# Performance work log

Hardware: AMD Instinct MI355X
Metric: run time of the kernel (lower is better)

The kernel has to match this reference:

```python
import jax, jax.numpy as jnp
import numpy as np

VOC, EMB, HID = 32000, 1024, 1024
B, S = 32, 128


def setup_inputs() -> dict:
    key = jax.random.key(0)
    ks = jax.random.split(key, 12)
    s_e = 1.0 / np.sqrt(EMB)
    s_h = 1.0 / np.sqrt(HID)
    return {
        "inputs": jax.random.randint(ks[0], (B, S), 0, VOC, dtype=jnp.int64),
        "emb": jax.random.normal(ks[1], (VOC, EMB), jnp.float32),
        "W_ih1": jax.random.uniform(ks[2], (4 * HID, EMB), jnp.float32, -s_h, s_h),
        "W_hh1": jax.random.uniform(ks[3], (4 * HID, HID), jnp.float32, -s_h, s_h),
        "b_ih1": jax.random.uniform(ks[4], (4 * HID,), jnp.float32, -s_h, s_h),
        "b_hh1": jax.random.uniform(ks[5], (4 * HID,), jnp.float32, -s_h, s_h),
        "W_ih2": jax.random.uniform(ks[6], (4 * HID, HID), jnp.float32, -s_h, s_h),
        "W_hh2": jax.random.uniform(ks[7], (4 * HID, HID), jnp.float32, -s_h, s_h),
        "b_ih2": jax.random.uniform(ks[8], (4 * HID,), jnp.float32, -s_h, s_h),
        "b_hh2": jax.random.uniform(ks[9], (4 * HID,), jnp.float32, -s_h, s_h),
        "W_out": jax.random.uniform(ks[10], (VOC, HID), jnp.float32, -s_h, s_h),
        "b_out": jnp.zeros((VOC,), jnp.float32),  # init_weights zeroes logits bias
    }


def _lstm_cell(x, h, c, W_ih, W_hh, b_ih, b_hh):
    # torch LSTMCell gate order: i, f, g, o
    gates = x @ W_ih.T + b_ih + h @ W_hh.T + b_hh  # [B, 4H]
    i, f, g, o = jnp.split(gates, 4, axis=-1)
    c_new = jax.nn.sigmoid(f) * c + jax.nn.sigmoid(i) * jnp.tanh(g)
    h_new = jax.nn.sigmoid(o) * jnp.tanh(c_new)
    return h_new, c_new


def reference(inputs, emb, W_ih1, W_hh1, b_ih1, b_hh1, W_ih2, W_hh2, b_ih2, b_hh2, W_out, b_out):
    embed = emb[inputs]  # [B, S, E]
    bsz = embed.shape[0]
    hid = W_hh1.shape[1]
    init = (jnp.zeros((bsz, hid), embed.dtype), jnp.zeros((bsz, hid), embed.dtype),
            jnp.zeros((bsz, hid), embed.dtype), jnp.zeros((bsz, hid), embed.dtype))

    def step(carry, x_t):
        h1, c1, h2, c2 = carry
        h1, c1 = _lstm_cell(x_t, h1, c1, W_ih1, W_hh1, b_ih1, b_hh1)
        h2, c2 = _lstm_cell(h1, h2, c2, W_ih2, W_hh2, b_ih2, b_hh2)  # dropout = identity (eval)
        return (h1, c1, h2, c2), h2

    _, hid_seq = jax.lax.scan(step, init, jnp.swapaxes(embed, 0, 1))  # [S, B, H]
    hid_seq = jnp.swapaxes(hid_seq, 0, 1)  # [B, S, H]
    logits = hid_seq @ W_out.T + b_out  # [B, S, V]
    return jax.nn.log_softmax(logits, axis=-1)
```

## Files before the change

### kernel.cpp

```cpp
#include <hip/hip_runtime.h>


#define SEQ   128
#define NBAT  32
#define HID   1024
#define VOC   32000

typedef __attribute__((ext_vector_type(4))) float        f32x4;
typedef __attribute__((ext_vector_type(4))) unsigned int u32x4;
typedef __attribute__((ext_vector_type(2))) unsigned int u32x2;

__device__ __forceinline__ unsigned short f2bf(float f) {
    unsigned u = __builtin_bit_cast(unsigned, f);
    u += 0x7fffu + ((u >> 16) & 1u);
    return (unsigned short)(u >> 16);
}
__device__ __forceinline__ unsigned pk2(float a, float b) {
    return (unsigned)f2bf(a) | ((unsigned)f2bf(b) << 16);
}
__device__ __forceinline__ void mfma16(f32x4& d, u32x4 a, u32x4 b) {
    asm("v_mfma_f32_16x16x32_bf16 %0, %1, %2, %0" : "+v"(d) : "v"(a), "v"(b));
}
__device__ __forceinline__ void mfma_fence() {
    __builtin_amdgcn_sched_barrier(0);
    asm volatile("s_nop 7\ns_nop 7\ns_nop 7");
    __builtin_amdgcn_sched_barrier(0);
}

__global__ void cast_bf16_k(const float* __restrict__ in,
                            unsigned short* __restrict__ out, int n4) {
    int i = blockIdx.x * blockDim.x + threadIdx.x;
    int stride = gridDim.x * blockDim.x;
    for (; i < n4; i += stride) {
        f32x4 v = ((const f32x4*)in)[i];
        u32x2 p = { pk2(v.x, v.y), pk2(v.z, v.w) };
        ((u32x2*)out)[i] = p;
    }
}

__global__ void gather_k(const int* __restrict__ tok, const float* __restrict__ emb,
                         unsigned short* __restrict__ xe) {
    int row = blockIdx.x;
    int t   = tok[row];
    const f32x4* src = (const f32x4*)(emb + (size_t)t * HID);
    u32x2*       dst = (u32x2*)(xe + (size_t)row * HID);
    int i = threadIdx.x;
    f32x4 v = src[i];
    u32x2 p = { pk2(v.x, v.y), pk2(v.z, v.w) };
    dst[i] = p;
}

template<bool BF32>
__global__ __launch_bounds__(256, 2) void gemm_k(
    const unsigned short* __restrict__ A, const void* __restrict__ Bsrc,
    const float* __restrict__ bias1, const float* __restrict__ bias2,
    float* __restrict__ C, int N)
{
    __shared__ u32x4 As[128][8];
    __shared__ u32x4 Bs[128][8];
    const int tid  = threadIdx.x;
    const int lane = tid & 63, wid = tid >> 6;
    const int wm = (wid >> 1) * 64, wn = (wid & 1) * 64;
    const int m0 = blockIdx.x * 128, n0 = blockIdx.y * 128;
    const int r = tid >> 1, half = tid & 1;
    f32x4 acc[4][4] = {};

    const unsigned short* Ar = A + (size_t)(m0 + r) * HID + half * 32;
    for (int kt = 0; kt < HID / 64; ++kt) {
        const int k0 = kt * 64;
        {
            const u32x4* s = (const u32x4*)(Ar + k0);
            #pragma unroll
            for (int c = 0; c < 4; ++c)
                As[r][(half * 4 + c) ^ (r & 7)] = s[c];
        }
        if constexpr (!BF32) {
            const u32x4* s = (const u32x4*)((const unsigned short*)Bsrc +
                              (size_t)(n0 + r) * HID + half * 32 + k0);
            #pragma unroll
            for (int c = 0; c < 4; ++c)
                Bs[r][(half * 4 + c) ^ (r & 7)] = s[c];
        } else {
            const f32x4* s = (const f32x4*)((const float*)Bsrc +
                              (size_t)(n0 + r) * HID + half * 32 + k0);
            #pragma unroll
            for (int c = 0; c < 4; ++c) {
                f32x4 v0 = s[2 * c], v1 = s[2 * c + 1];
                u32x4 p = { pk2(v0.x, v0.y), pk2(v0.z, v0.w),
                            pk2(v1.x, v1.y), pk2(v1.z, v1.w) };
                Bs[r][(half * 4 + c) ^ (r & 7)] = p;
            }
        }
        __syncthreads();
        #pragma unroll
        for (int h = 0; h < 2; ++h) {
            u32x4 af[4], bfr[4];
            #pragma unroll
            for (int i = 0; i < 4; ++i) {
                int ra = wm + i * 16 + (lane & 15);
                af[i]  = As[ra][(h * 4 + (lane >> 4)) ^ (ra & 7)];
                int rb = wn + i * 16 + (lane & 15);
                bfr[i] = Bs[rb][(h * 4 + (lane >> 4)) ^ (rb & 7)];
            }
            #pragma unroll
            for (int i = 0; i < 4; ++i)
                #pragma unroll
                for (int j = 0; j < 4; ++j)
                    mfma16(acc[i][j], af[i], bfr[j]);
        }
        __syncthreads();
    }
    mfma_fence();
    #pragma unroll
    for (int j = 0; j < 4; ++j) {
        int col = n0 + wn + j * 16 + (lane & 15);
        float bv = 0.f;
        if (bias1) bv += bias1[col];
        if (bias2) bv += bias2[col];
        #pragma unroll
        for (int i = 0; i < 4; ++i) {
            int mrow = m0 + wm + i * 16 + (lane >> 4) * 4;
            #pragma unroll
            for (int q = 0; q < 4; ++q)
                C[(size_t)(mrow + q) * N + col] = acc[i][j][q] + bv;
        }
    }
}

__global__ __launch_bounds__(256, 2) void lstm_k(
    const float* __restrict__ X, const unsigned short* __restrict__ Whh,
    unsigned short* __restrict__ hseq, float* __restrict__ cst, int t)
{
    __shared__ u32x4 hl[32][128];
    __shared__ float gl[4][32][16];
    const int tid  = threadIdx.x;
    const int lane = tid & 63, wid = tid >> 6;
    const int u0 = blockIdx.x * 16;
    f32x4 acc0 = {}, acc1 = {};

    if (t > 0) {
        const int b = tid >> 3;
        const u32x4* src = (const u32x4*)(hseq + (size_t)(b * SEQ + t - 1) * HID);
        #pragma unroll
        for (int q = 0; q < 16; ++q) {
            int c = (tid & 7) + q * 8;
            hl[b][c ^ (b & 7)] = src[c];
        }
        __syncthreads();
        const unsigned short* Wr = Whh + (size_t)(wid * HID + u0 + (lane & 15)) * HID
                                       + (lane >> 4) * 8;
        #pragma unroll 8
        for (int ks = 0; ks < 32; ++ks) {
            u32x4 bf = *(const u32x4*)(Wr + ks * 32);
            u32x4 a0 = hl[lane & 15][(ks * 4 + (lane >> 4)) ^ (lane & 7)];
            u32x4 a1 = hl[16 + (lane & 15)][(ks * 4 + (lane >> 4)) ^ (lane & 7)];
            mfma16(acc0, a0, bf);
            mfma16(acc1, a1, bf);
        }
    }
    mfma_fence();
    #pragma unroll
    for (int q = 0; q < 4; ++q) {
        gl[wid][(lane >> 4) * 4 + q][lane & 15]      = acc0[q];
        gl[wid][16 + (lane >> 4) * 4 + q][lane & 15] = acc1[q];
    }
    __syncthreads();
    #pragma unroll
    for (int p = tid; p < 512; p += 256) {
        const int b = p >> 4, u = p & 15;
        const float* Xr = X + (size_t)(b * SEQ + t) * (4 * HID) + u0 + u;
        float ig = gl[0][b][u] + Xr[0];
        float fg = gl[1][b][u] + Xr[HID];
        float gg = gl[2][b][u] + Xr[2 * HID];
        float og = gl[3][b][u] + Xr[3 * HID];
        float cp = (t == 0) ? 0.f : cst[b * HID + u0 + u];
        float si = 1.f / (1.f + __expf(-ig));
        float sf = 1.f / (1.f + __expf(-fg));
        float so = 1.f / (1.f + __expf(-og));
        float tg = tanhf(gg);
        float cn = sf * cp + si * tg;
        float hn = so * tanhf(cn);
        cst[b * HID + u0 + u] = cn;
        hseq[(size_t)(b * SEQ + t) * HID + u0 + u] = f2bf(hn);
    }
}

__global__ __launch_bounds__(256) void lsm_k(float* __restrict__ out) {
    const int tid = threadIdx.x;
    float* p = out + (size_t)blockIdx.x * VOC;
    float m = -1e30f, s = 0.f;
    for (int i = tid; i < VOC / 4; i += 256) {
        f32x4 v = ((const f32x4*)p)[i];
        float vm = fmaxf(fmaxf(v.x, v.y), fmaxf(v.z, v.w));
        if (vm > m) { s *= __expf(m - vm); m = vm; }
        s += __expf(v.x - m) + __expf(v.y - m) + __expf(v.z - m) + __expf(v.w - m);
    }
    #pragma unroll
    for (int o = 32; o; o >>= 1) {
        float om = __shfl_xor(m, o), os = __shfl_xor(s, o);
        float M = fmaxf(m, om);
        s = s * __expf(m - M) + os * __expf(om - M);
        m = M;
    }
    __shared__ float rm[4], rs[4];
    if ((tid & 63) == 0) { rm[tid >> 6] = m; rs[tid >> 6] = s; }
    __syncthreads();
    float M = fmaxf(fmaxf(rm[0], rm[1]), fmaxf(rm[2], rm[3]));
    float S = rs[0] * __expf(rm[0] - M) + rs[1] * __expf(rm[1] - M)
            + rs[2] * __expf(rm[2] - M) + rs[3] * __expf(rm[3] - M);
    float lse = M + logf(S);
    for (int i = tid; i < VOC / 4; i += 256) {
        f32x4 v = ((const f32x4*)p)[i];
        v.x -= lse; v.y -= lse; v.z -= lse; v.w -= lse;
        ((f32x4*)p)[i] = v;
    }
}

extern "C" void kernel_launch(void* const* d_in, const int* in_sizes, int n_in,
                              void* d_out, int out_size, void* d_ws, size_t ws_size,
                              hipStream_t stream)
{
    (void)in_sizes; (void)n_in; (void)out_size; (void)ws_size;
    const int*   tok  = (const int*)d_in[0];
    const float* emb  = (const float*)d_in[1];
    const float* Wih1 = (const float*)d_in[2];
    const float* Whh1 = (const float*)d_in[3];
    const float* bih1 = (const float*)d_in[4];
    const float* bhh1 = (const float*)d_in[5];
    const float* Wih2 = (const float*)d_in[6];
    const float* Whh2 = (const float*)d_in[7];
    const float* bih2 = (const float*)d_in[8];
    const float* bhh2 = (const float*)d_in[9];
    const float* Wout = (const float*)d_in[10];
    const float* bout = (const float*)d_in[11];
    float* out = (float*)d_out;
    char*  ws  = (char*)d_ws;

    unsigned short* Wih1b = (unsigned short*)(ws + (0ull  << 20));
    unsigned short* Whh1b = (unsigned short*)(ws + (8ull  << 20));
    unsigned short* Wih2b = (unsigned short*)(ws + (16ull << 20));
    unsigned short* Whh2b = (unsigned short*)(ws + (24ull << 20));
    unsigned short* Xemb  = (unsigned short*)(ws + (32ull << 20));
    unsigned short* h1s   = (unsigned short*)(ws + (40ull << 20));
    unsigned short* h2s   = (unsigned short*)(ws + (48ull << 20));
    float* c1 = (float*)(ws + (56ull << 20));
    float* c2 = (float*)(ws + (56ull << 20) + (1ull << 19));
    float* X1 = out;
    float* X2 = out + (16ull << 20);

    const int n4w = (4 * HID * HID) / 4;
    cast_bf16_k<<<1024, 256, 0, stream>>>(Wih1, Wih1b, n4w);
    cast_bf16_k<<<1024, 256, 0, stream>>>(Whh1, Whh1b, n4w);
    cast_bf16_k<<<1024, 256, 0, stream>>>(Wih2, Wih2b, n4w);
    cast_bf16_k<<<1024, 256, 0, stream>>>(Whh2, Whh2b, n4w);
    gather_k<<<NBAT * SEQ, 256, 0, stream>>>(tok, emb, Xemb);

    gemm_k<false><<<dim3(32, 32), 256, 0, stream>>>(Xemb, Wih1b, bih1, bhh1, X1, 4 * HID);
    for (int t = 0; t < SEQ; ++t)
        lstm_k<<<64, 256, 0, stream>>>(X1, Whh1b, h1s, c1, t);

    gemm_k<false><<<dim3(32, 32), 256, 0, stream>>>(h1s, Wih2b, bih2, bhh2, X2, 4 * HID);
    for (int t = 0; t < SEQ; ++t)
        lstm_k<<<64, 256, 0, stream>>>(X2, Whh2b, h2s, c2, t);

    gemm_k<true><<<dim3(32, VOC / 128), 256, 0, stream>>>(h2s, Wout, bout, nullptr, out, VOC);
    lsm_k<<<NBAT * SEQ, 256, 0, stream>>>(out);
}
```

Measured before the change: 3.677 ms.

## Replace per-timestep LSTM launches with persistent kernel and grid barrier

Each LSTM layer's 128 per-timestep launches are replaced by one persistent kernel of 128 blocks that loops over time, synchronised by an atomic counter grid barrier. Each block keeps its W_hh slice in registers as bf16, casting from fp32 at kernel start, so the separate W_hh cast kernels go away. The cell state stays in a register and h is read straight from global memory instead of being staged through LDS. This targets launch overhead and repeated weight reloads. In exchange it depends on all 128 blocks being co-resident for the spin barrier, and it uses heavy register pressure (128 VGPRs of weights).

```diff
diff --git a/kernel.cpp b/kernel.cpp
--- a/kernel.cpp
+++ b/kernel.cpp
@@ -5,6 +5,7 @@
 #define NBAT  32
 #define HID   1024
 #define VOC   32000
+#define RBLK  128
 
 typedef __attribute__((ext_vector_type(4))) float        f32x4;
 typedef __attribute__((ext_vector_type(4))) unsigned int u32x4;
@@ -127,61 +128,82 @@
     }
 }
 
-__global__ __launch_bounds__(256, 2) void lstm_k(
-    const float* __restrict__ X, const unsigned short* __restrict__ Whh,
-    unsigned short* __restrict__ hseq, float* __restrict__ cst, int t)
+__global__ __launch_bounds__(256, 1) void lstm_pers(
+    const float* __restrict__ X, const float* __restrict__ Whh,
+    unsigned short* __restrict__ hseq, unsigned* __restrict__ bar)
 {
-    __shared__ u32x4 hl[32][128];
-    __shared__ float gl[4][32][16];
+    __shared__ float gl[32][33];
     const int tid  = threadIdx.x;
     const int lane = tid & 63, wid = tid >> 6;
-    const int u0 = blockIdx.x * 16;
-    f32x4 acc0 = {}, acc1 = {};
-
-    if (t > 0) {
-        const int b = tid >> 3;
-        const u32x4* src = (const u32x4*)(hseq + (size_t)(b * SEQ + t - 1) * HID);
+    const int m    = wid & 1;
+    const int nh   = wid >> 1;
+    const int u0   = blockIdx.x * 8;
+
+    const int n    = nh * 16 + (lane & 15);
+    const int grow = (n >> 3) * HID + u0 + (n & 7);
+    const float* wr = Whh + (size_t)grow * HID + (lane >> 4) * 8;
+    u32x4 wreg[32];
+    #pragma unroll
+    for (int kk = 0; kk < 32; ++kk) {
+        f32x4 v0 = *(const f32x4*)(wr + kk * 32);
+        f32x4 v1 = *(const f32x4*)(wr + kk * 32 + 4);
+        u32x4 p = { pk2(v0.x, v0.y), pk2(v0.z, v0.w),
+                    pk2(v1.x, v1.y), pk2(v1.z, v1.w) };
+        wreg[kk] = p;
+    }
+
+    const unsigned short* hbase = hseq +
+        (size_t)(m * 16 + (lane & 15)) * SEQ * HID + (lane >> 4) * 8;
+
+    const int batch = tid >> 3, j = tid & 7;
+    const float* xb = X + (size_t)(batch * SEQ) * (4 * HID) + u0 + j;
+    unsigned short* hw = hseq + (size_t)(batch * SEQ) * HID + u0 + j;
+    float creg = 0.f;
+
+    for (int t = 0; t < SEQ; ++t) {
+        f32x4 acc_a = {}, acc_b = {};
+        if (t > 0) {
+            const unsigned short* hp = hbase + (size_t)(t - 1) * HID;
+            #pragma unroll
+            for (int kk = 0; kk < 32; kk += 2) {
+                u32x4 a0 = *(const u32x4*)(hp + kk * 32);
+                u32x4 a1 = *(const u32x4*)(hp + kk * 32 + 32);
+                mfma16(acc_a, a0, wreg[kk]);
+                mfma16(acc_b, a1, wreg[kk + 1]);
+            }
+        }
+        mfma_fence();
         #pragma unroll
-        for (int q = 0; q < 16; ++q) {
-            int c = (tid & 7) + q * 8;
-            hl[b][c ^ (b & 7)] = src[c];
-        }
+        for (int q = 0; q < 4; ++q)
+            gl[m * 16 + (lane >> 4) * 4 + q][nh * 16 + (lane & 15)]
+                = acc_a[q] + acc_b[q];
         __syncthreads();
-        const unsigned short* Wr = Whh + (size_t)(wid * HID + u0 + (lane & 15)) * HID
-                                       + (lane >> 4) * 8;
-        #pragma unroll 8
-        for (int ks = 0; ks < 32; ++ks) {
-            u32x4 bf = *(const u32x4*)(Wr + ks * 32);
-            u32x4 a0 = hl[lane & 15][(ks * 4 + (lane >> 4)) ^ (lane & 7)];
-            u32x4 a1 = hl[16 + (lane & 15)][(ks * 4 + (lane >> 4)) ^ (lane & 7)];
-            mfma16(acc0, a0, bf);
-            mfma16(acc1, a1, bf);
-        }
-    }
-    mfma_fence();
-    #pragma unroll
-    for (int q = 0; q < 4; ++q) {
-        gl[wid][(lane >> 4) * 4 + q][lane & 15]      = acc0[q];
-        gl[wid][16 + (lane >> 4) * 4 + q][lane & 15] = acc1[q];
-    }
-    __syncthreads();
-    #pragma unroll
-    for (int p = tid; p < 512; p += 256) {
-        const int b = p >> 4, u = p & 15;
-        const float* Xr = X + (size_t)(b * SEQ + t) * (4 * HID) + u0 + u;
-        float ig = gl[0][b][u] + Xr[0];
-        float fg = gl[1][b][u] + Xr[HID];
-        float gg = gl[2][b][u] + Xr[2 * HID];
-        float og = gl[3][b][u] + Xr[3 * HID];
-        float cp = (t == 0) ? 0.f : cst[b * HID + u0 + u];
-        float si = 1.f / (1.f + __expf(-ig));
-        float sf = 1.f / (1.f + __expf(-fg));
-        float so = 1.f / (1.f + __expf(-og));
-        float tg = tanhf(gg);
-        float cn = sf * cp + si * tg;
-        float hn = so * tanhf(cn);
-        cst[b * HID + u0 + u] = cn;
-        hseq[(size_t)(b * SEQ + t) * HID + u0 + u] = f2bf(hn);
+        {
+            const float* Xr = xb + (size_t)t * (4 * HID);
+            float ig = gl[batch][j]      + Xr[0];
+            float fg = gl[batch][8 + j]  + Xr[HID];
+            float gg = gl[batch][16 + j] + Xr[2 * HID];
+            float og = gl[batch][24 + j] + Xr[3 * HID];
+            float si = 1.f / (1.f + __expf(-ig));
+            float sf = 1.f / (1.f + __expf(-fg));
+            float so = 1.f / (1.f + __expf(-og));
+            float tg = tanhf(gg);
+            creg = sf * creg + si * tg;
+            hw[(size_t)t * HID] = f2bf(so * tanhf(creg));
+        }
+        if (t < SEQ - 1) {
+            __syncthreads();
+            if (tid == 0) {
+                __hip_atomic_fetch_add(bar, 1u, __ATOMIC_RELEASE,
+                                       __HIP_MEMORY_SCOPE_AGENT);
+                const unsigned target = (unsigned)(t + 1) * (unsigned)gridDim.x;
+                while (__hip_atomic_load(bar, __ATOMIC_RELAXED,
+                                         __HIP_MEMORY_SCOPE_AGENT) < target)
+                    __builtin_amdgcn_s_sleep(2);
+                __threadfence();
+            }
+            __syncthreads();
+        }
     }
 }
 
@@ -237,31 +259,26 @@
     char*  ws  = (char*)d_ws;
 
     unsigned short* Wih1b = (unsigned short*)(ws + (0ull  << 20));
-    unsigned short* Whh1b = (unsigned short*)(ws + (8ull  << 20));
-    unsigned short* Wih2b = (unsigned short*)(ws + (16ull << 20));
-    unsigned short* Whh2b = (unsigned short*)(ws + (24ull << 20));
-    unsigned short* Xemb  = (unsigned short*)(ws + (32ull << 20));
-    unsigned short* h1s   = (unsigned short*)(ws + (40ull << 20));
-    unsigned short* h2s   = (unsigned short*)(ws + (48ull << 20));
-    float* c1 = (float*)(ws + (56ull << 20));
-    float* c2 = (float*)(ws + (56ull << 20) + (1ull << 19));
+    unsigned short* Wih2b = (unsigned short*)(ws + (8ull  << 20));
+    unsigned short* Xemb  = (unsigned short*)(ws + (16ull << 20));
+    unsigned short* h1s   = (unsigned short*)(ws + (24ull << 20));
+    unsigned short* h2s   = (unsigned short*)(ws + (32ull << 20));
+    unsigned*       bar   = (unsigned*)(ws + (40ull << 20));
     float* X1 = out;
     float* X2 = out + (16ull << 20);
 
     const int n4w = (4 * HID * HID) / 4;
     cast_bf16_k<<<1024, 256, 0, stream>>>(Wih1, Wih1b, n4w);
-    cast_bf16_k<<<1024, 256, 0, stream>>>(Whh1, Whh1b, n4w);
     cast_bf16_k<<<1024, 256, 0, stream>>>(Wih2, Wih2b, n4w);
-    cast_bf16_k<<<1024, 256, 0, stream>>>(Whh2, Whh2b, n4w);
     gather_k<<<NBAT * SEQ, 256, 0, stream>>>(tok, emb, Xemb);
 
     gemm_k<false><<<dim3(32, 32), 256, 0, stream>>>(Xemb, Wih1b, bih1, bhh1, X1, 4 * HID);
-    for (int t = 0; t < SEQ; ++t)
-        lstm_k<<<64, 256, 0, stream>>>(X1, Whh1b, h1s, c1, t);
+    hipMemsetAsync(bar, 0, 128, stream);
+    lstm_pers<<<RBLK, 256, 0, stream>>>(X1, Whh1, h1s, bar);
 
     gemm_k<false><<<dim3(32, 32), 256, 0, stream>>>(h1s, Wih2b, bih2, bhh2, X2, 4 * HID);
-    for (int t = 0; t < SEQ; ++t)
-        lstm_k<<<64, 256, 0, stream>>>(X2, Whh2b, h2s, c2, t);
+    hipMemsetAsync(bar, 0, 128, stream);
+    lstm_pers<<<RBLK, 256, 0, stream>>>(X2, Whh2, h2s, bar);
 
     gemm_k<true><<<dim3(32, VOC / 128), 256, 0, stream>>>(h2s, Wout, bout, nullptr, out, VOC);
     lsm_k<<<NBAT * SEQ, 256, 0, stream>>>(out);
```

Measured after the change: 5.112 ms. 39.0% more time.
